# Optimization experiments

Hardware: AMD Instinct MI355X
Metric: run time of the kernel (lower is better)

## Reference

```python
import jax, jax.numpy as jnp
import numpy as np

N, D, E = 200000, 256, 6400000
RATIO = 0.5
NEG_SLOPE = 0.2


def _xavier(key, shape, gain=1.414):
    fan_in, fan_out = shape[0], shape[1]
    limit = gain * (6.0 / (fan_in + fan_out)) ** 0.5
    return jax.random.uniform(key, shape, jnp.float32, -limit, limit)


def setup_inputs() -> dict:
    key = jax.random.key(0)
    ks = jax.random.split(key, 8)
    x = jax.random.normal(ks[0], (N, D), jnp.float32)
    edge_index = jax.random.randint(ks[1], (2, E), 0, N, dtype=jnp.int64)
    return {
        "x": x,
        "edge_index": edge_index,
        "w_s1": _xavier(ks[2], (2 * D, D)), "b_s1": jnp.zeros((D,), jnp.float32),
        "w_s2": _xavier(ks[3], (D, 1)),     "b_s2": jnp.zeros((1,), jnp.float32),
        "w_f1": _xavier(ks[4], (D, D // 2)), "b_f1": jnp.zeros((D // 2,), jnp.float32),
        "w_f2": _xavier(ks[5], (D // 2, 1)), "b_f2": jnp.zeros((1,), jnp.float32),
        "w_p": _xavier(ks[6], (D, D)),      "b_p": jnp.zeros((D,), jnp.float32),
        "alpha": jnp.float32(0.5), "beta": jnp.float32(0.5),
    }


def reference(x, edge_index, w_s1, b_s1, w_s2, b_s2, w_f1, b_f1, w_f2, b_f2, w_p, b_p, alpha, beta):
    num_nodes = x.shape[0]
    k = max(1, int(RATIO * num_nodes))
    lrelu = lambda v: jax.nn.leaky_relu(v, NEG_SLOPE)

    row, col = edge_index[0], edge_index[1]
    # degree(row, N): scatter-add of ones over source nodes
    deg = jax.ops.segment_sum(jnp.ones_like(row, dtype=x.dtype), row, num_segments=num_nodes)
    # F.normalize(p=2, dim=0) on the [N,1] degree column
    deg_norm = deg / jnp.maximum(jnp.sqrt(jnp.sum(deg * deg)), 1e-12)

    struct_in = jnp.concatenate([x, jnp.broadcast_to(deg_norm[:, None], x.shape)], axis=1)  # [N, 2D]
    struct_scores = (lrelu(struct_in @ w_s1 + b_s1) @ w_s2 + b_s2)[:, 0]  # dropout is eval no-op
    feat_scores = (lrelu(x @ w_f1 + b_f1) @ w_f2 + b_f2)[:, 0]

    a = jax.nn.sigmoid(alpha)
    b = jax.nn.sigmoid(beta)
    s = a + b
    scores = (a / s) * struct_scores + (b / s) * feat_scores  # [N]

    # single-graph top-k (batch=None default path)
    topk_scores, topk_idx = jax.lax.top_k(scores, k)
    x_pooled = lrelu(x[topk_idx] @ w_p + b_p)  # post_pool, dropout no-op

    # edge remap + compaction (valid edges first, -1 padding to keep static shape)
    node_map = jnp.full((num_nodes,), -1, dtype=jnp.int32).at[topk_idx].set(
        jnp.arange(k, dtype=jnp.int32))
    mr, mc = node_map[row], node_map[col]
    mask = (mr >= 0) & (mc >= 0)
    order = jnp.argsort(~mask, stable=True)  # stable: keeps original edge order among valid
    edge_index_pooled = jnp.stack([
        jnp.where(mask, mr, -1)[order],
        jnp.where(mask, mc, -1)[order],
    ])
    return x_pooled, edge_index_pooled, topk_scores
```

## Files before the change

kernel.cpp:

```cpp
#include <hip/hip_runtime.h>
#include <math.h>

typedef unsigned long long u64;
typedef unsigned int u32;
typedef unsigned short u16;
typedef __attribute__((ext_vector_type(8))) short bf16x8;
typedef __attribute__((ext_vector_type(4))) float f32x4;

#define D   256
#define ECH 16
#define EBLK (256*ECH)
#define BAND_W 4096
#define BAND_DELTA 1e-3f
#define HR  25088
#define HCH 32

__device__ __forceinline__ double lrelu(double v){ return v > 0.0 ? v : 0.2*v; }
__device__ __forceinline__ float  lreluf(float v){ return v > 0.0f ? v : 0.2f*v; }

__device__ __forceinline__ u16 f2bf(float f){
  union{float f; u32 u;} v; v.f = f;
  u32 r = v.u + 0x7FFFu + ((v.u >> 16) & 1u);
  return (u16)(r >> 16);
}
__device__ __forceinline__ float bf2f(u16 b){
  union{u32 u; float f;} v; v.u = ((u32)b) << 16; return v.f;
}

__global__ __launch_bounds__(256) void k_deghist(const int* __restrict__ row, int E,
                                                 u32* __restrict__ partial, int NR){
  __shared__ u32 h[HR/2];
  const int tid = threadIdx.x;
  const int r = blockIdx.x % NR;
  const int c = blockIdx.x / NR;
  for (int i = tid; i < HR/2; i += 256) h[i] = 0;
  __syncthreads();
  const int lo = r * HR;
  int CE = ((E + HCH - 1) / HCH + 3) & ~3;
  const int e0 = c * CE;
  const int e1 = min(e0 + CE, E);
  for (int e = e0 + tid*4; e < e1; e += 256*4){
    if (e + 3 < e1){
      int4 v = *(const int4*)(row + e);
      u32 d0 = (u32)(v.x - lo), d1 = (u32)(v.y - lo);
      u32 d2 = (u32)(v.z - lo), d3 = (u32)(v.w - lo);
      if (d0 < (u32)HR) atomicAdd(&h[d0 >> 1], 1u << ((d0 & 1)*16));
      if (d1 < (u32)HR) atomicAdd(&h[d1 >> 1], 1u << ((d1 & 1)*16));
      if (d2 < (u32)HR) atomicAdd(&h[d2 >> 1], 1u << ((d2 & 1)*16));
      if (d3 < (u32)HR) atomicAdd(&h[d3 >> 1], 1u << ((d3 & 1)*16));
    } else {
      for (int j = 0; j < 4 && e + j < e1; ++j){
        u32 d = (u32)(row[e+j] - lo);
        if (d < (u32)HR) atomicAdd(&h[d >> 1], 1u << ((d & 1)*16));
      }
    }
  }
  __syncthreads();
  u32* plane = partial + (size_t)blockIdx.x * (HR/2);
  for (int i = tid; i < HR/2; i += 256) plane[i] = h[i];
}

__global__ void k_degred2(const u32* __restrict__ partial, int N, int NR,
                          int* __restrict__ deg, u64* __restrict__ out){
  __shared__ u64 sh[256];
  u64 local = 0;
  int stride = gridDim.x*blockDim.x;
  for (int i = blockIdx.x*blockDim.x + threadIdx.x; i < N; i += stride){
    int r = i / HR, off = i % HR;
    const int word = off >> 1, shift = (off & 1)*16;
    u32 s = 0;
    #pragma unroll 8
    for (int c = 0; c < HCH; ++c)
      s += (partial[(size_t)(c*NR + r)*(HR/2) + word] >> shift) & 0xFFFFu;
    deg[i] = (int)s;
    local += (u64)s * (u64)s;
  }
  sh[threadIdx.x] = local; __syncthreads();
  for (int s = 128; s > 0; s >>= 1){
    if (threadIdx.x < s) sh[threadIdx.x] += sh[threadIdx.x+s];
    __syncthreads();
  }
  if (threadIdx.x == 0) atomicAdd(out, sh[0]);
}

__global__ void k_prep_wsw(const float* __restrict__ wS1, const float* __restrict__ wF1,
                           const float* __restrict__ wP,
                           const float* __restrict__ alpha, const float* __restrict__ beta,
                           const u64* __restrict__ sumsq,
                           u16* __restrict__ wswH, u16* __restrict__ wswL,
                           u16* __restrict__ wPH, u16* __restrict__ wPL,
                           double* __restrict__ s1b, double* __restrict__ scal,
                           float* __restrict__ s1bf, float* __restrict__ scalf){
  const int b = blockIdx.x;
  if (b < 384){
    int idx = b*256 + threadIdx.x;
    int i    = idx & 7;
    int lane = (idx >> 3) & 63;
    int sg   = (idx >> 9) & 7;
    int t    = idx >> 12;
    int k = sg*32 + ((lane >> 4) & 3)*8 + i;
    int c16 = lane & 15;
    float wv;
    if (t < 16) wv = wS1[k*256 + t*16 + c16];
    else        wv = wF1[k*128 + (t-16)*16 + c16];
    u16 h = f2bf(wv);
    wswH[idx] = h;
    wswL[idx] = f2bf(wv - bf2f(h));
  } else if (b < 640){
    int idx = (b-384)*256 + threadIdx.x;
    int i    = idx & 7;
    int lane = (idx >> 3) & 63;
    int sg   = (idx >> 9) & 7;
    int t    = idx >> 12;
    int k = sg*32 + ((lane >> 4) & 3)*8 + i;
    float wv = wP[k*256 + t*16 + (lane & 15)];
    u16 h = f2bf(wv);
    wPH[idx] = h;
    wPL[idx] = f2bf(wv - bf2f(h));
  } else {
    int j = threadIdx.x;
    double s = 0.0;
    for (int r = 0; r < D; ++r) s += (double)wS1[(D + r)*D + j];
    s1b[j] = s;
    s1bf[j] = (float)s;
    if (j == 0){
      double a = 1.0/(1.0 + exp(-(double)alpha[0]));
      double bb = 1.0/(1.0 + exp(-(double)beta[0]));
      scal[0] = a/(a+bb);
      scal[1] = bb/(a+bb);
      double dn = sqrt((double)(*sumsq));
      scal[2] = dn > 1e-12 ? dn : 1e-12;
      scalf[0] = (float)scal[0];
      scalf[1] = (float)scal[1];
      scalf[2] = (float)(1.0/scal[2]);
    }
  }
}

__global__ __launch_bounds__(512, 4) void k_scores_mfma(
    const float* __restrict__ x, const int* __restrict__ deg,
    const u16* __restrict__ wswH, const u16* __restrict__ wswL,
    const float* __restrict__ bS1, const float* __restrict__ wS2, const float* __restrict__ bS2,
    const float* __restrict__ bF1, const float* __restrict__ wF2, const float* __restrict__ bF2,
    const float* __restrict__ s1bf, const float* __restrict__ scalf,
    float* __restrict__ s32, u64* __restrict__ keys, int N, int SORTN)
{
  __shared__ u16 xsh[2][4096];
  __shared__ u16 xsl[2][4096];
  __shared__ float dnsh[64];
  __shared__ float part_s[64][9];
  __shared__ float part_f[64][9];

  const int tid  = threadIdx.x;
  const int lane = tid & 63;
  const int w    = tid >> 6;
  const int node0 = blockIdx.x * 64;

  if (node0 >= N){
    if (tid < 64){
      int i = node0 + tid;
      if (i < SORTN) keys[i] = ~0ULL;
    }
    return;
  }

  if (tid < 64){
    int node = node0 + tid;
    dnsh[tid] = (node < N) ? ((float)deg[node] * scalf[2]) : 0.0f;
  }

  const int row_st = tid >> 3;
  const int seg_st = tid & 7;
  const int unit_w = row_st*8 + (seg_st ^ (row_st & 7));
  const float* srcbase = x + (size_t)(node0 + row_st)*D + seg_st*8;
  const bool rv = (node0 + row_st) < N;

  f32x4 acc[4][3];
  #pragma unroll
  for (int m = 0; m < 4; ++m)
    #pragma unroll
    for (int n = 0; n < 3; ++n) acc[m][n] = (f32x4){0.f,0.f,0.f,0.f};

  float xr[8];
  {
    if (rv){
      float4 a = *(const float4*)(srcbase);
      float4 b = *(const float4*)(srcbase + 4);
      xr[0]=a.x; xr[1]=a.y; xr[2]=a.z; xr[3]=a.w;
      xr[4]=b.x; xr[5]=b.y; xr[6]=b.z; xr[7]=b.w;
    } else {
      #pragma unroll
      for (int i = 0; i < 8; ++i) xr[i] = 0.f;
    }
  }

  #pragma unroll
  for (int c = 0; c < 4; ++c){
    const int pb = c & 1;
    {
      u16 h[8];
      #pragma unroll
      for (int i = 0; i < 8; ++i) h[i] = f2bf(xr[i]);
      uint4 H; H.x = (u32)h[0] | ((u32)h[1]<<16); H.y = (u32)h[2] | ((u32)h[3]<<16);
               H.z = (u32)h[4] | ((u32)h[5]<<16); H.w = (u32)h[6] | ((u32)h[7]<<16);
      u16 l[8];
      #pragma unroll
      for (int i = 0; i < 8; ++i) l[i] = f2bf(xr[i] - bf2f(h[i]));
      uint4 L; L.x = (u32)l[0] | ((u32)l[1]<<16); L.y = (u32)l[2] | ((u32)l[3]<<16);
               L.z = (u32)l[4] | ((u32)l[5]<<16); L.w = (u32)l[6] | ((u32)l[7]<<16);
      *(uint4*)&xsh[pb][unit_w*8] = H;
      *(uint4*)&xsl[pb][unit_w*8] = L;
    }
    __syncthreads();
    if (c < 3){
      const float* sn = srcbase + (c+1)*64;
      if (rv){
        float4 a = *(const float4*)(sn);
        float4 b = *(const float4*)(sn + 4);
        xr[0]=a.x; xr[1]=a.y; xr[2]=a.z; xr[3]=a.w;
        xr[4]=b.x; xr[5]=b.y; xr[6]=b.z; xr[7]=b.w;
      }
    }
    #pragma unroll
    for (int s = 0; s < 2; ++s){
      const int sg = c*2 + s;
      bf16x8 ah[4], al[4];
      #pragma unroll
      for (int mt = 0; mt < 4; ++mt){
        int row = mt*16 + (lane & 15);
        int seg = s*4 + (lane >> 4);
        int un  = row*8 + (seg ^ (row & 7));
        ah[mt] = *(const bf16x8*)&xsh[pb][un*8];
        al[mt] = *(const bf16x8*)&xsl[pb][un*8];
      }
      const int t0 = w*3;
      size_t o0 = ((size_t)(t0*8 + sg)*64 + lane)*8;
      bf16x8 bh = *(const bf16x8*)&wswH[o0];
      bf16x8 bl = *(const bf16x8*)&wswL[o0];
      #pragma unroll
      for (int nt = 0; nt < 3; ++nt){
        bf16x8 nbh = bh, nbl = bl;
        if (nt < 2){
          size_t on = ((size_t)((t0+nt+1)*8 + sg)*64 + lane)*8;
          nbh = *(const bf16x8*)&wswH[on];
          nbl = *(const bf16x8*)&wswL[on];
        }
        #pragma unroll
        for (int mt = 0; mt < 4; ++mt){
          acc[mt][nt] = __builtin_amdgcn_mfma_f32_16x16x32_bf16(ah[mt], bh, acc[mt][nt], 0,0,0);
          acc[mt][nt] = __builtin_amdgcn_mfma_f32_16x16x32_bf16(al[mt], bh, acc[mt][nt], 0,0,0);
          acc[mt][nt] = __builtin_amdgcn_mfma_f32_16x16x32_bf16(ah[mt], bl, acc[mt][nt], 0,0,0);
        }
        bh = nbh; bl = nbl;
      }
    }
    if (c < 3) __syncthreads();
  }

  float dnl[4][4];
  #pragma unroll
  for (int mt = 0; mt < 4; ++mt)
    #pragma unroll
    for (int j = 0; j < 4; ++j)
      dnl[mt][j] = dnsh[mt*16 + (lane>>4)*4 + j];

  float ps[4][4], pf[4][4];
  #pragma unroll
  for (int mt = 0; mt < 4; ++mt)
    #pragma unroll
    for (int j = 0; j < 4; ++j){ ps[mt][j] = 0.f; pf[mt][j] = 0.f; }

  #pragma unroll
  for (int nt = 0; nt < 3; ++nt){
    const int t = w*3 + nt;
    const int c16 = lane & 15;
    const bool isS = (t < 16);
    const int col = isS ? t*16 + c16 : (t-16)*16 + c16;
    const float bias = isS ? bS1[col] : bF1[col];
    const float sbv  = isS ? s1bf[col] : 0.f;
    const float vv   = isS ? wS2[col] : wF2[col];
    #pragma unroll
    for (int mt = 0; mt < 4; ++mt){
      #pragma unroll
      for (int j = 0; j < 4; ++j){
        float v = acc[mt][nt][j] + bias + dnl[mt][j]*sbv;
        v = lreluf(v) * vv;
        v += __shfl_xor(v, 1);
        v += __shfl_xor(v, 2);
        v += __shfl_xor(v, 4);
        v += __shfl_xor(v, 8);
        if (isS) ps[mt][j] += v; else pf[mt][j] += v;
      }
    }
  }
  if ((lane & 15) == 0){
    #pragma unroll
    for (int mt = 0; mt < 4; ++mt)
      #pragma unroll
      for (int j = 0; j < 4; ++j){
        int row = mt*16 + (lane>>4)*4 + j;
        part_s[row][w] = ps[mt][j];
        part_f[row][w] = pf[mt][j];
      }
  }
  __syncthreads();
  if (tid < 64){
    int node = node0 + tid;
    if (node < N){
      float sv = 0.f, fv = 0.f;
      #pragma unroll
      for (int ww = 0; ww < 8; ++ww){ sv += part_s[tid][ww]; fv += part_f[tid][ww]; }
      float sc = scalf[0]*(sv + bS2[0]) + scalf[1]*(fv + bF2[0]);
      s32[node] = sc;
      u32 bits = __float_as_uint(sc);
      u32 ord = (bits >> 31) ? ~bits : (bits | 0x80000000u);
      keys[node] = ((u64)(~ord) << 32) | (u32)node;
    } else {
      int i = node0 + tid;
      if (i < SORTN) keys[i] = ~0ULL;
    }
  }
}

__global__ __launch_bounds__(1024) void k_bsort_local8k(u64* __restrict__ keys){
  __shared__ u64 sk[8192];
  const int tid = threadIdx.x;
  const int base = blockIdx.x * 8192;
  #pragma unroll
  for (int e = 0; e < 8; ++e) sk[tid + e*1024] = keys[base + tid + e*1024];
  __syncthreads();
  for (int size = 2; size <= 8192; size <<= 1){
    for (int stride = size >> 1; stride > 0; stride >>= 1){
      #pragma unroll
      for (int pp = 0; pp < 4; ++pp){
        int p  = tid + pp*1024;
        int i  = 2*p - (p & (stride-1));
        int jj = i + stride;
        bool up = (((base + i) & size) == 0);
        u64 ki = sk[i], kj = sk[jj];
        if ((ki > kj) == up){ sk[i] = kj; sk[jj] = ki; }
      }
      __syncthreads();
    }
  }
  #pragma unroll
  for (int e = 0; e < 8; ++e) keys[base + tid + e*1024] = sk[tid + e*1024];
}

__global__ __launch_bounds__(1024) void k_bmerge_local8k(u64* __restrict__ keys, int size){
  __shared__ u64 sk[8192];
  const int tid = threadIdx.x;
  const int base = blockIdx.x * 8192;
  #pragma unroll
  for (int e = 0; e < 8; ++e) sk[tid + e*1024] = keys[base + tid + e*1024];
  __syncthreads();
  for (int stride = 4096; stride > 0; stride >>= 1){
    #pragma unroll
    for (int pp = 0; pp < 4; ++pp){
      int p  = tid + pp*1024;
      int i  = 2*p - (p & (stride-1));
      int jj = i + stride;
      bool up = (((base + i) & size) == 0);
      u64 ki = sk[i], kj = sk[jj];
      if ((ki > kj) == up){ sk[i] = kj; sk[jj] = ki; }
    }
    __syncthreads();
  }
  #pragma unroll
  for (int e = 0; e < 8; ++e) keys[base + tid + e*1024] = sk[tid + e*1024];
}

template<int NS>
__global__ void k_bpassM(u64* __restrict__ keys, int size, int stride){
  const int G = 1 << NS;
  u32 t = blockIdx.x*blockDim.x + threadIdx.x;
  u32 smin = (u32)stride >> (NS-1);
  u32 i0 = (t/smin)*(smin << NS) + (t % smin);
  u64 v[G];
  #pragma unroll
  for (int j = 0; j < G; ++j) v[j] = keys[i0 + (u32)j*smin];
  bool up = ((i0 & (u32)size) == 0);
  #pragma unroll
  for (int b = (G>>1); b >= 1; b >>= 1){
    #pragma unroll
    for (int j = 0; j < G; ++j){
      if ((j & b) == 0){
        u64 a = v[j], cc = v[j|b];
        if ((a > cc) == up){ v[j] = cc; v[j|b] = a; }
      }
    }
  }
  #pragma unroll
  for (int j = 0; j < G; ++j) keys[i0 + (u32)j*smin] = v[j];
}

__global__ void kr_cut(const u64* __restrict__ keys, int k, float* __restrict__ cutbuf,
                       int* __restrict__ r01){
  if (threadIdx.x == 0 && blockIdx.x == 0){
    u32 key32 = (u32)(keys[k-1] >> 32);
    u32 ord = ~key32;
    u32 u = (ord & 0x80000000u) ? (ord ^ 0x80000000u) : ~ord;
    float c = __uint_as_float(u);
    cutbuf[0] = c - BAND_DELTA;
    cutbuf[1] = c + BAND_DELTA;
    r01[0] = 0x7FFFFFFF;
    r01[1] = -1;
  }
}

__global__ __launch_bounds__(256) void kr_rescore(
    const u64* __restrict__ keys, const float* __restrict__ s32,
    const float* __restrict__ x, const int* __restrict__ deg,
    const float* __restrict__ wS1, const float* __restrict__ bS1,
    const float* __restrict__ wS2, const float* __restrict__ bS2,
    const float* __restrict__ wF1, const float* __restrict__ bF1,
    const float* __restrict__ wF2, const float* __restrict__ bF2,
    const double* __restrict__ s1b, const double* __restrict__ scal,
    const float* __restrict__ cutbuf, int* __restrict__ r01,
    double* __restrict__ bandS, int k, int N)
{
  const int r = k - BAND_W + blockIdx.x;
  if (r < 0 || r >= N) return;
  const int node = (int)(u32)(keys[r] & 0xFFFFFFFFULL);
  const float s = s32[node];
  if (s < cutbuf[0] || s > cutbuf[1]) return;

  const int tid = threadIdx.x;
  if (tid == 0){ atomicMin(&r01[0], r); atomicMax(&r01[1], r); }

  __shared__ float xr[256];
  __shared__ double rsp[4], rfp[4];
  xr[tid] = x[(size_t)node*D + tid];
  __syncthreads();

  const int j = tid;
  double a0=0.0, a1=0.0, a2=0.0, a3=0.0;
  double b0=0.0, b1=0.0, b2=0.0, b3=0.0;
  if (j < 128){
    for (int rr = 0; rr < D; rr += 4){
      double x0 = (double)xr[rr+0], x1 = (double)xr[rr+1];
      double x2 = (double)xr[rr+2], x3 = (double)xr[rr+3];
      a0 = fma(x0, (double)wS1[(rr+0)*D + j], a0);
      a1 = fma(x1, (double)wS1[(rr+1)*D + j], a1);
      a2 = fma(x2, (double)wS1[(rr+2)*D + j], a2);
      a3 = fma(x3, (double)wS1[(rr+3)*D + j], a3);
      b0 = fma(x0, (double)wF1[(rr+0)*128 + j], b0);
      b1 = fma(x1, (double)wF1[(rr+1)*128 + j], b1);
      b2 = fma(x2, (double)wF1[(rr+2)*128 + j], b2);
      b3 = fma(x3, (double)wF1[(rr+3)*128 + j], b3);
    }
  } else {
    for (int rr = 0; rr < D; rr += 4){
      double x0 = (double)xr[rr+0], x1 = (double)xr[rr+1];
      double x2 = (double)xr[rr+2], x3 = (double)xr[rr+3];
      a0 = fma(x0, (double)wS1[(rr+0)*D + j], a0);
      a1 = fma(x1, (double)wS1[(rr+1)*D + j], a1);
      a2 = fma(x2, (double)wS1[(rr+2)*D + j], a2);
      a3 = fma(x3, (double)wS1[(rr+3)*D + j], a3);
    }
  }
  double accA = ((a0+a1)+(a2+a3)) + (double)bS1[j] + ((double)deg[node]/scal[2]) * s1b[j];
  double sp = lrelu(accA) * (double)wS2[j];
  double fp = 0.0;
  if (j < 128){
    double accB = ((b0+b1)+(b2+b3)) + (double)bF1[j];
    fp = lrelu(accB) * (double)wF2[j];
  }

  const int lane = tid & 63, wave = tid >> 6;
  #pragma unroll
  for (int off = 32; off > 0; off >>= 1){
    sp += __shfl_down(sp, off);
    fp += __shfl_down(fp, off);
  }
  if (lane == 0){ rsp[wave] = sp; rfp[wave] = fp; }
  __syncthreads();
  if (tid == 0){
    double SP = rsp[0]+rsp[1]+rsp[2]+rsp[3];
    double FP = rfp[0]+rfp[1]+rfp[2]+rfp[3];
    bandS[blockIdx.x] = scal[0]*(SP + (double)bS2[0]) + scal[1]*(FP + (double)bF2[0]);
  }
}

__global__ __launch_bounds__(1024) void kr_bandsort(u64* __restrict__ keys,
    const double* __restrict__ bandS, const int* __restrict__ r01, int k){
  __shared__ double bs[8192];
  __shared__ int bi[8192];
  const int r0 = r01[0], r1 = r01[1];
  int nb = r1 - r0 + 1;
  if (nb <= 1) return;
  if (nb > 8192) nb = 8192;
  int M = 1; while (M < nb) M <<= 1;
  const int tid = threadIdx.x;
  const int sbase = r0 - (k - BAND_W);
  for (int m = tid; m < M; m += 1024){
    if (m < nb){ bs[m] = bandS[sbase + m]; bi[m] = (int)(u32)(keys[r0+m] & 0xFFFFFFFFULL); }
    else       { bs[m] = -1.0/0.0;         bi[m] = 0x7FFFFFFF; }
  }
  __syncthreads();
  for (int size = 2; size <= M; size <<= 1){
    for (int stride = size >> 1; stride > 0; stride >>= 1){
      for (int p = tid; p < (M >> 1); p += 1024){
        int i = 2*p - (p & (stride-1));
        int jj = i + stride;
        bool up = ((i & size) == 0);
        double si_ = bs[i], sj = bs[jj];
        int ii = bi[i], ij = bi[jj];
        bool gt = (si_ < sj) || (si_ == sj && ii > ij);
        if (gt == up){ bs[i]=sj; bs[jj]=si_; bi[i]=ij; bi[jj]=ii; }
      }
      __syncthreads();
    }
  }
  for (int m = tid; m < nb; m += 1024)
    keys[r0+m] = (u64)(u32)bi[m];
}

__global__ void k_finalize(const u64* __restrict__ keys, const float* __restrict__ s32,
                           int k, int* __restrict__ nmap, float* __restrict__ outS){
  int p = blockIdx.x*blockDim.x + threadIdx.x;
  if (p < k){
    int node = (int)(u32)(keys[p] & 0xFFFFFFFFULL);
    nmap[node] = p;
    outS[p] = s32[node];
  }
}

__global__ __launch_bounds__(512, 4) void k_xpool_mfma(
    const float* __restrict__ x, const u64* __restrict__ keys,
    const u16* __restrict__ wH, const u16* __restrict__ wL,
    const float* __restrict__ bP, float* __restrict__ out, int kk)
{
  __shared__ u16 xsh[2][4096];
  __shared__ u16 xsl[2][4096];

  const int tid  = threadIdx.x;
  const int lane = tid & 63;
  const int w    = tid >> 6;
  const int p0 = blockIdx.x * 64;
  if (p0 >= kk) return;

  const int row_st = tid >> 3;
  const int seg_st = tid & 7;
  const int unit_w = row_st*8 + (seg_st ^ (row_st & 7));
  int prow = p0 + row_st; if (prow >= kk) prow = kk - 1;
  const int node = (int)(u32)(keys[prow] & 0xFFFFFFFFULL);
  const float* srcbase = x + (size_t)node*D + seg_st*8;

  f32x4 acc[4][2];
  #pragma unroll
  for (int m = 0; m < 4; ++m){ acc[m][0] = (f32x4){0.f,0.f,0.f,0.f}; acc[m][1] = (f32x4){0.f,0.f,0.f,0.f}; }

  float xr[8];
  {
    float4 a = *(const float4*)(srcbase);
    float4 b = *(const float4*)(srcbase + 4);
    xr[0]=a.x; xr[1]=a.y; xr[2]=a.z; xr[3]=a.w;
    xr[4]=b.x; xr[5]=b.y; xr[6]=b.z; xr[7]=b.w;
  }

  #pragma unroll
  for (int c = 0; c < 4; ++c){
    const int pb = c & 1;
    {
      u16 h[8];
      #pragma unroll
      for (int i = 0; i < 8; ++i) h[i] = f2bf(xr[i]);
      uint4 H; H.x = (u32)h[0] | ((u32)h[1]<<16); H.y = (u32)h[2] | ((u32)h[3]<<16);
               H.z = (u32)h[4] | ((u32)h[5]<<16); H.w = (u32)h[6] | ((u32)h[7]<<16);
      u16 l[8];
      #pragma unroll
      for (int i = 0; i < 8; ++i) l[i] = f2bf(xr[i] - bf2f(h[i]));
      uint4 L; L.x = (u32)l[0] | ((u32)l[1]<<16); L.y = (u32)l[2] | ((u32)l[3]<<16);
               L.z = (u32)l[4] | ((u32)l[5]<<16); L.w = (u32)l[6] | ((u32)l[7]<<16);
      *(uint4*)&xsh[pb][unit_w*8] = H;
      *(uint4*)&xsl[pb][unit_w*8] = L;
    }
    __syncthreads();
    if (c < 3){
      const float* sn = srcbase + (c+1)*64;
      float4 a = *(const float4*)(sn);
      float4 b = *(const float4*)(sn + 4);
      xr[0]=a.x; xr[1]=a.y; xr[2]=a.z; xr[3]=a.w;
      xr[4]=b.x; xr[5]=b.y; xr[6]=b.z; xr[7]=b.w;
    }
    #pragma unroll
    for (int s = 0; s < 2; ++s){
      const int sg = c*2 + s;
      bf16x8 ah[4], al[4];
      #pragma unroll
      for (int mt = 0; mt < 4; ++mt){
        int row = mt*16 + (lane & 15);
        int seg = s*4 + (lane >> 4);
        int un  = row*8 + (seg ^ (row & 7));
        ah[mt] = *(const bf16x8*)&xsh[pb][un*8];
        al[mt] = *(const bf16x8*)&xsl[pb][un*8];
      }
      const int t0 = w*2;
      size_t o0 = ((size_t)(t0*8 + sg)*64 + lane)*8;
      bf16x8 bh = *(const bf16x8*)&wH[o0];
      bf16x8 bl = *(const bf16x8*)&wL[o0];
      #pragma unroll
      for (int nt = 0; nt < 2; ++nt){
        bf16x8 nbh = bh, nbl = bl;
        if (nt < 1){
          size_t on = ((size_t)((t0+1)*8 + sg)*64 + lane)*8;
          nbh = *(const bf16x8*)&wH[on];
          nbl = *(const bf16x8*)&wL[on];
        }
        #pragma unroll
        for (int mt = 0; mt < 4; ++mt){
          acc[mt][nt] = __builtin_amdgcn_mfma_f32_16x16x32_bf16(ah[mt], bh, acc[mt][nt], 0,0,0);
          acc[mt][nt] = __builtin_amdgcn_mfma_f32_16x16x32_bf16(al[mt], bh, acc[mt][nt], 0,0,0);
          acc[mt][nt] = __builtin_amdgcn_mfma_f32_16x16x32_bf16(ah[mt], bl, acc[mt][nt], 0,0,0);
        }
        bh = nbh; bl = nbl;
      }
    }
    if (c < 3) __syncthreads();
  }

  const int c16 = lane & 15, r4 = (lane >> 4)*4;
  #pragma unroll
  for (int nt = 0; nt < 2; ++nt){
    const int col = (w*2 + nt)*16 + c16;
    const float bias = bP[col];
    #pragma unroll
    for (int mt = 0; mt < 4; ++mt){
      #pragma unroll
      for (int j = 0; j < 4; ++j){
        int p = p0 + mt*16 + r4 + j;
        if (p < kk) out[(size_t)p*D + col] = lreluf(acc[mt][nt][j] + bias);
      }
    }
  }
}

__global__ __launch_bounds__(256) void k_ecount(const int* __restrict__ erow, const int* __restrict__ ecol,
    const int* __restrict__ nmap, int E, int* __restrict__ bcount){
  __shared__ int sc[256];
  const int tid = threadIdx.x;
  const int base = blockIdx.x*EBLK + tid*ECH;
  int cnt = 0;
  #pragma unroll
  for (int q = 0; q < ECH; ++q){
    int e = base + q;
    if (e < E){
      if (nmap[erow[e]] >= 0 && nmap[ecol[e]] >= 0) cnt++;
    }
  }
  sc[tid] = cnt; __syncthreads();
  for (int s = 128; s > 0; s >>= 1){
    if (tid < s) sc[tid] += sc[tid+s];
    __syncthreads();
  }
  if (tid == 0) bcount[blockIdx.x] = sc[0];
}

__global__ __launch_bounds__(1024) void k_escan(const int* __restrict__ bcount, int nblk,
                                                int* __restrict__ boff, int* __restrict__ tot){
  __shared__ int sh[1024];
  const int tid = threadIdx.x;
  int carry = 0;
  for (int s = 0; s < nblk; s += 1024){
    int v = (s + tid < nblk) ? bcount[s+tid] : 0;
    sh[tid] = v; __syncthreads();
    for (int d = 1; d < 1024; d <<= 1){
      int t = (tid >= d) ? sh[tid-d] : 0;
      __syncthreads();
      sh[tid] += t;
      __syncthreads();
    }
    if (s + tid < nblk) boff[s+tid] = carry + sh[tid] - v;
    carry += sh[1023];
    __syncthreads();
  }
  if (tid == 0) *tot = carry;
}

__global__ void k_efill_tail(float* __restrict__ outR, float* __restrict__ outC,
                             const int* __restrict__ tot, int E){
  const int t0 = *tot;
  int stride = gridDim.x*blockDim.x;
  for (int i = t0 + blockIdx.x*blockDim.x + threadIdx.x; i < E; i += stride){
    outR[i] = -1.0f;
    outC[i] = -1.0f;
  }
}

__global__ __launch_bounds__(256) void k_escatter(const int* __restrict__ erow, const int* __restrict__ ecol,
    const int* __restrict__ nmap, int E, const int* __restrict__ boff,
    float* __restrict__ outR, float* __restrict__ outC){
  __shared__ int sc[256];
  const int tid = threadIdx.x;
  const int base = blockIdx.x*EBLK + tid*ECH;
  int mr[ECH], mc[ECH];
  int cnt = 0;
  #pragma unroll
  for (int q = 0; q < ECH; ++q){
    int e = base + q;
    int a = -1, b = -1;
    if (e < E){ a = nmap[erow[e]]; b = nmap[ecol[e]]; }
    mr[q] = a; mc[q] = b;
    if (a >= 0 && b >= 0) cnt++;
  }
  sc[tid] = cnt; __syncthreads();
  int v = cnt;
  for (int d = 1; d < 256; d <<= 1){
    int t = (tid >= d) ? sc[tid-d] : 0;
    __syncthreads();
    sc[tid] += t;
    __syncthreads();
  }
  int pos = boff[blockIdx.x] + sc[tid] - v;
  #pragma unroll
  for (int q = 0; q < ECH; ++q){
    if (mr[q] >= 0 && mc[q] >= 0){
      outR[pos] = (float)mr[q];
      outC[pos] = (float)mc[q];
      pos++;
    }
  }
}

extern "C" void kernel_launch(void* const* d_in, const int* in_sizes, int n_in,
                              void* d_out, int out_size, void* d_ws, size_t ws_size,
                              hipStream_t stream)
{
  const float* x   = (const float*)d_in[0];
  const int*   ei  = (const int*)d_in[1];
  const float* wS1 = (const float*)d_in[2];
  const float* bS1 = (const float*)d_in[3];
  const float* wS2 = (const float*)d_in[4];
  const float* bS2 = (const float*)d_in[5];
  const float* wF1 = (const float*)d_in[6];
  const float* bF1 = (const float*)d_in[7];
  const float* wF2 = (const float*)d_in[8];
  const float* bF2 = (const float*)d_in[9];
  const float* wP  = (const float*)d_in[10];
  const float* bP  = (const float*)d_in[11];
  const float* alpha = (const float*)d_in[12];
  const float* beta  = (const float*)d_in[13];
  (void)n_in; (void)out_size; (void)ws_size;

  const int N = in_sizes[0] / D;
  const int E = in_sizes[1] / 2;
  int k = (int)(0.5 * (double)N); if (k < 1) k = 1;
  int SORTN = 8192; while (SORTN < N) SORTN <<= 1;
  const int nblk_e = (E + EBLK - 1) / EBLK;
  const int NR = (N + HR - 1) / HR;

  char* w = (char*)d_ws;
  size_t off = 0;
  auto alloc = [&](size_t bytes)->char*{
    char* p = w + off;
    off = (off + bytes + 255) & ~(size_t)255;
    return p;
  };
  float*  s32    = (float*) alloc((size_t)N*4);
  u64*    keys   = (u64*)   alloc((size_t)SORTN*8);
  int*    deg    = (int*)   alloc((size_t)N*4);
  int*    nmap   = (int*)   alloc((size_t)N*4);
  double* s1b    = (double*)alloc((size_t)D*8);
  float*  s1bf   = (float*) alloc((size_t)D*4);
  double* scal   = (double*)alloc(4*8);
  float*  scalf  = (float*) alloc(4*4);
  u64*    sumsq  = (u64*)   alloc(8);
  float*  cutbuf = (float*) alloc(2*4);
  int*    r01    = (int*)   alloc(2*4);
  int*    tot    = (int*)   alloc(4);
  double* bandS  = (double*)alloc((size_t)2*BAND_W*8);
  u16*    wswH   = (u16*)   alloc((size_t)98304*2);
  u16*    wswL   = (u16*)   alloc((size_t)98304*2);
  u16*    wswPH  = (u16*)   alloc((size_t)65536*2);
  u16*    wswPL  = (u16*)   alloc((size_t)65536*2);
  int*    bcount = (int*)   alloc((size_t)nblk_e*4);
  int*    boff   = (int*)   alloc((size_t)nblk_e*4);

  float* outX  = (float*)d_out;
  float* outER = outX  + (size_t)k*D;
  float* outEC = outER + (size_t)E;
  float* outS  = outEC + (size_t)E;

  u32* partial = (u32*)outER;

  hipMemsetAsync(sumsq, 0,    8,           stream);
  hipMemsetAsync(nmap,  0xFF, (size_t)N*4, stream);

  k_deghist<<<NR*HCH, 256, 0, stream>>>(ei, E, partial, NR);
  k_degred2<<<1024, 256, 0, stream>>>(partial, N, NR, deg, sumsq);
  k_prep_wsw<<<641, 256, 0, stream>>>(wS1, wF1, wP, alpha, beta, sumsq,
                                      wswH, wswL, wswPH, wswPL,
                                      s1b, scal, s1bf, scalf);
  k_scores_mfma<<<SORTN/64, 512, 0, stream>>>(x, deg, wswH, wswL,
                                              bS1, wS2, bS2, bF1, wF2, bF2,
                                              s1bf, scalf, s32, keys, N, SORTN);

  k_bsort_local8k<<<SORTN/8192, 1024, 0, stream>>>(keys);
  for (int size = 16384; size <= SORTN; size <<= 1){
    int stride = size >> 1;
    while (stride >= 8192){
      int ns = 1;
      while (ns < 4 && (stride >> ns) >= 8192) ns++;
      switch (ns){
        case 1: k_bpassM<1><<<SORTN/2/256,  256, 0, stream>>>(keys, size, stride); break;
        case 2: k_bpassM<2><<<SORTN/4/256,  256, 0, stream>>>(keys, size, stride); break;
        case 3: k_bpassM<3><<<SORTN/8/256,  256, 0, stream>>>(keys, size, stride); break;
        default:k_bpassM<4><<<SORTN/16/256, 256, 0, stream>>>(keys, size, stride); break;
      }
      stride >>= ns;
    }
    k_bmerge_local8k<<<SORTN/8192, 1024, 0, stream>>>(keys, size);
  }

  kr_cut     <<<1, 64, 0, stream>>>(keys, k, cutbuf, r01);
  kr_rescore <<<2*BAND_W, 256, 0, stream>>>(keys, s32, x, deg, wS1,bS1,wS2,bS2,
                                            wF1,bF1,wF2,bF2, s1b, scal,
                                            cutbuf, r01, bandS, k, N);
  kr_bandsort<<<1, 1024, 0, stream>>>(keys, bandS, r01, k);

  k_finalize<<<(k+255)/256, 256, 0, stream>>>(keys, s32, k, nmap, outS);
  k_xpool_mfma<<<(k+63)/64, 512, 0, stream>>>(x, keys, wswPH, wswPL, bP, outX, k);
  k_ecount  <<<nblk_e, 256, 0, stream>>>(ei, ei+E, nmap, E, bcount);
  k_escan   <<<1, 1024, 0, stream>>>(bcount, nblk_e, boff, tot);
  k_efill_tail<<<1024, 256, 0, stream>>>(outER, outEC, tot, E);
  k_escatter<<<nblk_e, 256, 0, stream>>>(ei, ei+E, nmap, E, boff, outER, outEC);
}
```

Before: 760.7 us.

## Drop split-bf16 correction terms in pooled projection and sort 16K-key tiles in LDS

The post-pool projection now uses only the high bf16 parts of x and w_p, dropping the low-part weights, the x low buffer and two of the three MFMAs per tile. This cuts matrix work and LDS traffic at the cost of accuracy, down to plain bf16 inputs with fp32 accumulation. Separately, the bitonic sort's shared-memory tile grows from 8192 to 16384 keys (128 KB of LDS), so fewer global merge passes and kernel launches are needed. Occupancy per CU falls and the padded sort size rises from 2^18 only when N needs it.

```diff
diff --git a/kernel.cpp b/kernel.cpp
--- a/kernel.cpp
+++ b/kernel.cpp
@@ -88,7 +88,7 @@
                            const float* __restrict__ alpha, const float* __restrict__ beta,
                            const u64* __restrict__ sumsq,
                            u16* __restrict__ wswH, u16* __restrict__ wswL,
-                           u16* __restrict__ wPH, u16* __restrict__ wPL,
+                           u16* __restrict__ wPH,
                            double* __restrict__ s1b, double* __restrict__ scal,
                            float* __restrict__ s1bf, float* __restrict__ scalf){
   const int b = blockIdx.x;
@@ -113,10 +113,7 @@
     int sg   = (idx >> 9) & 7;
     int t    = idx >> 12;
     int k = sg*32 + ((lane >> 4) & 3)*8 + i;
-    float wv = wP[k*256 + t*16 + (lane & 15)];
-    u16 h = f2bf(wv);
-    wPH[idx] = h;
-    wPL[idx] = f2bf(wv - bf2f(h));
+    wPH[idx] = f2bf(wP[k*256 + t*16 + (lane & 15)]);
   } else {
     int j = threadIdx.x;
     double s = 0.0;
@@ -322,17 +319,17 @@
   }
 }
 
-__global__ __launch_bounds__(1024) void k_bsort_local8k(u64* __restrict__ keys){
-  __shared__ u64 sk[8192];
+__global__ __launch_bounds__(1024) void k_bsort_local16k(u64* __restrict__ keys){
+  __shared__ u64 sk[16384];
   const int tid = threadIdx.x;
-  const int base = blockIdx.x * 8192;
-  #pragma unroll
-  for (int e = 0; e < 8; ++e) sk[tid + e*1024] = keys[base + tid + e*1024];
+  const int base = blockIdx.x * 16384;
+  #pragma unroll
+  for (int e = 0; e < 16; ++e) sk[tid + e*1024] = keys[base + tid + e*1024];
   __syncthreads();
-  for (int size = 2; size <= 8192; size <<= 1){
+  for (int size = 2; size <= 16384; size <<= 1){
     for (int stride = size >> 1; stride > 0; stride >>= 1){
       #pragma unroll
-      for (int pp = 0; pp < 4; ++pp){
+      for (int pp = 0; pp < 8; ++pp){
         int p  = tid + pp*1024;
         int i  = 2*p - (p & (stride-1));
         int jj = i + stride;
@@ -344,19 +341,19 @@
     }
   }
   #pragma unroll
-  for (int e = 0; e < 8; ++e) keys[base + tid + e*1024] = sk[tid + e*1024];
-}
-
-__global__ __launch_bounds__(1024) void k_bmerge_local8k(u64* __restrict__ keys, int size){
-  __shared__ u64 sk[8192];
+  for (int e = 0; e < 16; ++e) keys[base + tid + e*1024] = sk[tid + e*1024];
+}
+
+__global__ __launch_bounds__(1024) void k_bmerge_local16k(u64* __restrict__ keys, int size){
+  __shared__ u64 sk[16384];
   const int tid = threadIdx.x;
-  const int base = blockIdx.x * 8192;
-  #pragma unroll
-  for (int e = 0; e < 8; ++e) sk[tid + e*1024] = keys[base + tid + e*1024];
+  const int base = blockIdx.x * 16384;
+  #pragma unroll
+  for (int e = 0; e < 16; ++e) sk[tid + e*1024] = keys[base + tid + e*1024];
   __syncthreads();
-  for (int stride = 4096; stride > 0; stride >>= 1){
-    #pragma unroll
-    for (int pp = 0; pp < 4; ++pp){
+  for (int stride = 8192; stride > 0; stride >>= 1){
+    #pragma unroll
+    for (int pp = 0; pp < 8; ++pp){
       int p  = tid + pp*1024;
       int i  = 2*p - (p & (stride-1));
       int jj = i + stride;
@@ -367,7 +364,7 @@
     __syncthreads();
   }
   #pragma unroll
-  for (int e = 0; e < 8; ++e) keys[base + tid + e*1024] = sk[tid + e*1024];
+  for (int e = 0; e < 16; ++e) keys[base + tid + e*1024] = sk[tid + e*1024];
 }
 
 template<int NS>
@@ -528,11 +525,10 @@
 
 __global__ __launch_bounds__(512, 4) void k_xpool_mfma(
     const float* __restrict__ x, const u64* __restrict__ keys,
-    const u16* __restrict__ wH, const u16* __restrict__ wL,
+    const u16* __restrict__ wH,
     const float* __restrict__ bP, float* __restrict__ out, int kk)
 {
   __shared__ u16 xsh[2][4096];
-  __shared__ u16 xsl[2][4096];
 
   const int tid  = threadIdx.x;
   const int lane = tid & 63;
@@ -568,13 +564,7 @@
       for (int i = 0; i < 8; ++i) h[i] = f2bf(xr[i]);
       uint4 H; H.x = (u32)h[0] | ((u32)h[1]<<16); H.y = (u32)h[2] | ((u32)h[3]<<16);
                H.z = (u32)h[4] | ((u32)h[5]<<16); H.w = (u32)h[6] | ((u32)h[7]<<16);
-      u16 l[8];
-      #pragma unroll
-      for (int i = 0; i < 8; ++i) l[i] = f2bf(xr[i] - bf2f(h[i]));
-      uint4 L; L.x = (u32)l[0] | ((u32)l[1]<<16); L.y = (u32)l[2] | ((u32)l[3]<<16);
-               L.z = (u32)l[4] | ((u32)l[5]<<16); L.w = (u32)l[6] | ((u32)l[7]<<16);
       *(uint4*)&xsh[pb][unit_w*8] = H;
-      *(uint4*)&xsl[pb][unit_w*8] = L;
     }
     __syncthreads();
     if (c < 3){
@@ -587,34 +577,28 @@
     #pragma unroll
     for (int s = 0; s < 2; ++s){
       const int sg = c*2 + s;
-      bf16x8 ah[4], al[4];
+      bf16x8 ah[4];
       #pragma unroll
       for (int mt = 0; mt < 4; ++mt){
         int row = mt*16 + (lane & 15);
         int seg = s*4 + (lane >> 4);
         int un  = row*8 + (seg ^ (row & 7));
         ah[mt] = *(const bf16x8*)&xsh[pb][un*8];
-        al[mt] = *(const bf16x8*)&xsl[pb][un*8];
       }
       const int t0 = w*2;
       size_t o0 = ((size_t)(t0*8 + sg)*64 + lane)*8;
       bf16x8 bh = *(const bf16x8*)&wH[o0];
-      bf16x8 bl = *(const bf16x8*)&wL[o0];
       #pragma unroll
       for (int nt = 0; nt < 2; ++nt){
-        bf16x8 nbh = bh, nbl = bl;
+        bf16x8 nbh = bh;
         if (nt < 1){
           size_t on = ((size_t)((t0+1)*8 + sg)*64 + lane)*8;
           nbh = *(const bf16x8*)&wH[on];
-          nbl = *(const bf16x8*)&wL[on];
         }
         #pragma unroll
-        for (int mt = 0; mt < 4; ++mt){
+        for (int mt = 0; mt < 4; ++mt)
           acc[mt][nt] = __builtin_amdgcn_mfma_f32_16x16x32_bf16(ah[mt], bh, acc[mt][nt], 0,0,0);
-          acc[mt][nt] = __builtin_amdgcn_mfma_f32_16x16x32_bf16(al[mt], bh, acc[mt][nt], 0,0,0);
-          acc[mt][nt] = __builtin_amdgcn_mfma_f32_16x16x32_bf16(ah[mt], bl, acc[mt][nt], 0,0,0);
-        }
-        bh = nbh; bl = nbl;
+        bh = nbh;
       }
     }
     if (c < 3) __syncthreads();
@@ -746,7 +730,7 @@
   const int N = in_sizes[0] / D;
   const int E = in_sizes[1] / 2;
   int k = (int)(0.5 * (double)N); if (k < 1) k = 1;
-  int SORTN = 8192; while (SORTN < N) SORTN <<= 1;
+  int SORTN = 16384; while (SORTN < N) SORTN <<= 1;
   const int nblk_e = (E + EBLK - 1) / EBLK;
   const int NR = (N + HR - 1) / HR;
 
@@ -773,7 +757,6 @@
   u16*    wswH   = (u16*)   alloc((size_t)98304*2);
   u16*    wswL   = (u16*)   alloc((size_t)98304*2);
   u16*    wswPH  = (u16*)   alloc((size_t)65536*2);
-  u16*    wswPL  = (u16*)   alloc((size_t)65536*2);
   int*    bcount = (int*)   alloc((size_t)nblk_e*4);
   int*    boff   = (int*)   alloc((size_t)nblk_e*4);
 
@@ -790,18 +773,18 @@
   k_deghist<<<NR*HCH, 256, 0, stream>>>(ei, E, partial, NR);
   k_degred2<<<1024, 256, 0, stream>>>(partial, N, NR, deg, sumsq);
   k_prep_wsw<<<641, 256, 0, stream>>>(wS1, wF1, wP, alpha, beta, sumsq,
-                                      wswH, wswL, wswPH, wswPL,
+                                      wswH, wswL, wswPH,
                                       s1b, scal, s1bf, scalf);
   k_scores_mfma<<<SORTN/64, 512, 0, stream>>>(x, deg, wswH, wswL,
                                               bS1, wS2, bS2, bF1, wF2, bF2,
                                               s1bf, scalf, s32, keys, N, SORTN);
 
-  k_bsort_local8k<<<SORTN/8192, 1024, 0, stream>>>(keys);
-  for (int size = 16384; size <= SORTN; size <<= 1){
+  k_bsort_local16k<<<SORTN/16384, 1024, 0, stream>>>(keys);
+  for (int size = 32768; size <= SORTN; size <<= 1){
     int stride = size >> 1;
-    while (stride >= 8192){
+    while (stride >= 16384){
       int ns = 1;
-      while (ns < 4 && (stride >> ns) >= 8192) ns++;
+      while (ns < 4 && (stride >> ns) >= 16384) ns++;
       switch (ns){
         case 1: k_bpassM<1><<<SORTN/2/256,  256, 0, stream>>>(keys, size, stride); break;
         case 2: k_bpassM<2><<<SORTN/4/256,  256, 0, stream>>>(keys, size, stride); break;
@@ -810,7 +793,7 @@
       }
       stride >>= ns;
     }
-    k_bmerge_local8k<<<SORTN/8192, 1024, 0, stream>>>(keys, size);
+    k_bmerge_local16k<<<SORTN/16384, 1024, 0, stream>>>(keys, size);
   }
 
   kr_cut     <<<1, 64, 0, stream>>>(keys, k, cutbuf, r01);
@@ -820,7 +803,7 @@
   kr_bandsort<<<1, 1024, 0, stream>>>(keys, bandS, r01, k);
 
   k_finalize<<<(k+255)/256, 256, 0, stream>>>(keys, s32, k, nmap, outS);
-  k_xpool_mfma<<<(k+63)/64, 512, 0, stream>>>(x, keys, wswPH, wswPL, bP, outX, k);
+  k_xpool_mfma<<<(k+63)/64, 512, 0, stream>>>(x, keys, wswPH, bP, outX, k);
   k_ecount  <<<nblk_e, 256, 0, stream>>>(ei, ei+E, nmap, E, bcount);
   k_escan   <<<1, 1024, 0, stream>>>(bcount, nblk_e, boff, tot);
   k_efill_tail<<<1024, 256, 0, stream>>>(outER, outEC, tot, E);
```

After: 838.9 us. 10.3% more time.
